# Performance work log

Hardware: AMD Instinct MI355X
Metric: run time of the kernel (lower is better)

The kernel has to match this reference:

```python
import jax, jax.numpy as jnp
from jax import lax
import numpy as np

D, DI, S, K, R = 128, 256, 16, 4, 8  # d_model, d_inner, d_state, d_conv, dt_rank
B, W, N, E = 8, 64, 128, 256


def _ln(x, g, b, eps=1e-5):
    m = x.mean(-1, keepdims=True)
    v = ((x - m) ** 2).mean(-1, keepdims=True)
    return (x - m) * lax.rsqrt(v + eps) * g + b


def _mamba(x, w_in, conv_w, conv_b, w_xp, dt_w, dt_b, Alog, Dp, w_out):
    # x: (Bq, W, D) -> (Bq, W, D). Faithful mamba_ssm.Mamba math (selective scan).
    Bq, Wlen, _ = x.shape
    xz = x @ w_in                       # (Bq, W, 2*DI)
    xc, z = jnp.split(xz, 2, axis=-1)
    # causal depthwise conv over time
    xt = xc.transpose(0, 2, 1)          # (Bq, DI, W)
    xt = lax.conv_general_dilated(xt, conv_w[:, None, :], (1,), [(K - 1, 0)],
                                  feature_group_count=DI)
    xc = jax.nn.silu(xt + conv_b[None, :, None]).transpose(0, 2, 1)  # (Bq, W, DI)
    dbc = xc @ w_xp                     # (Bq, W, R+2S)
    dt = jax.nn.softplus(dbc[..., :R] @ dt_w + dt_b)   # (Bq, W, DI)
    Bm = dbc[..., R:R + S]              # (Bq, W, S)
    Cm = dbc[..., R + S:]               # (Bq, W, S)
    A = -jnp.exp(Alog)                  # (DI, S)

    def step(h, inp):
        dt_t, B_t, C_t, x_t = inp       # (Bq,DI),(Bq,S),(Bq,S),(Bq,DI)
        dA = jnp.exp(dt_t[..., None] * A)                 # (Bq,DI,S)
        h = dA * h + (dt_t * x_t)[..., None] * B_t[:, None, :]
        y = jnp.einsum('bds,bs->bd', h, C_t)
        return h, y

    h0 = jnp.zeros((Bq, DI, S), x.dtype)
    _, ys = lax.scan(step, h0, (dt.transpose(1, 0, 2), Bm.transpose(1, 0, 2),
                                Cm.transpose(1, 0, 2), xc.transpose(1, 0, 2)))
    y = ys.transpose(1, 0, 2) + xc * Dp          # D skip connection
    y = y * jax.nn.silu(z)
    return y @ w_out


def _forward(x_node, x_trace, x_log, mp_in, mp_conv_w, mp_conv_b, mp_xproj,
             mp_dt_w, mp_dt_b, mp_Alog, mp_D, mp_out, mix_w, mix_b,
             an_g, an_b, ff1_w, ff1_b, ff2_w, ff2_b, fln_g, fln_b):
    Bz, Wz, Nz, _ = x_node.shape
    Ez = x_trace.shape[2]
    # (B,W,N,D) -> (B*N, W, D) per-entity temporal sequences
    sn = x_node.transpose(0, 2, 1, 3).reshape(Bz * Nz, Wz, D)
    st = x_trace.transpose(0, 2, 1, 3).reshape(Bz * Ez, Wz, D)
    sl = x_log.transpose(0, 2, 1, 3).reshape(Bz * Nz, Wz, D)

    def mam(i, s):
        return _mamba(s, mp_in[i], mp_conv_w[i], mp_conv_b[i], mp_xproj[i],
                      mp_dt_w[i], mp_dt_b[i], mp_Alog[i], mp_D[i], mp_out[i])

    yn, yt, yl = mam(0, sn), mam(1, st), mam(2, sl)

    # cross-modal mixing of node & log with residual (dropout = identity in eval)
    cat = jnp.concatenate([yn, yl], axis=-1)          # (B*N, W, 2D)
    cat = cat + jax.nn.silu(cat @ mix_w + mix_b)
    yn, yl = jnp.split(cat, 2, axis=-1)

    # back to (B, W, N/E, D)
    yn = yn.reshape(Bz, Nz, Wz, D).transpose(0, 2, 1, 3)
    yt = yt.reshape(Bz, Ez, Wz, D).transpose(0, 2, 1, 3)
    yl = yl.reshape(Bz, Nz, Wz, D).transpose(0, 2, 1, 3)

    # AddALL: AddNorm(old, new) = LN(dropout(new) + old)
    n1 = _ln(yn + x_node, an_g[0], an_b[0])
    t1 = _ln(yt + x_trace, an_g[1], an_b[1])
    l1 = _ln(yl + x_log, an_g[2], an_b[2])

    # FFN: AddNorm(x, FeedForward(x)) per modality, LeakyReLU(0.01)
    def ffn(i, x):
        h = jax.nn.leaky_relu(x @ ff1_w[i] + ff1_b[i], 0.01)
        return _ln(h @ ff2_w[i] + ff2_b[i] + x, fln_g[i], fln_b[i])

    n2, t2, l2 = ffn(0, n1), ffn(1, t1), ffn(2, l1)
    # concat along entity axis (all feature dims = D) for a single output
    return jnp.concatenate([n2, t2, l2], axis=2)      # (B, W, 2N+E, D)


def setup_inputs() -> dict:
    key = jax.random.key(0)
    ks = jax.random.split(key, 16)
    f = lambda k, shp, s=1.0: jax.random.normal(k, shp, dtype=jnp.float32) * s
    return {
        'x_node': f(ks[0], (B, W, N, D)),
        'x_trace': f(ks[1], (B, W, E, D)),
        'x_log': f(ks[2], (B, W, N, D)),
        'mp_in': f(ks[3], (3, D, 2 * DI), 0.05),
        'mp_conv_w': f(ks[4], (3, DI, K), 0.2),
        'mp_conv_b': jnp.zeros((3, DI), jnp.float32),
        'mp_xproj': f(ks[5], (3, DI, R + 2 * S), 0.05),
        'mp_dt_w': f(ks[6], (3, R, DI), 0.1),
        'mp_dt_b': jnp.full((3, DI), float(np.log(np.expm1(0.01))), jnp.float32),
        'mp_Alog': jnp.log(jnp.broadcast_to(jnp.arange(1, S + 1, dtype=jnp.float32), (3, DI, S))),
        'mp_D': jnp.ones((3, DI), jnp.float32),
        'mp_out': f(ks[7], (3, DI, D), 0.05),
        'mix_w': f(ks[8], (2 * D, 2 * D), 0.05),
        'mix_b': jnp.zeros((2 * D,), jnp.float32),
        'an_g': jnp.ones((3, D), jnp.float32),
        'an_b': jnp.zeros((3, D), jnp.float32),
        'ff1_w': f(ks[9], (3, D, 4 * D), 0.05),
        'ff1_b': jnp.zeros((3, 4 * D), jnp.float32),
        'ff2_w': f(ks[10], (3, 4 * D, D), 0.05),
        'ff2_b': jnp.zeros((3, D), jnp.float32),
        'fln_g': jnp.ones((3, D), jnp.float32),
        'fln_b': jnp.zeros((3, D), jnp.float32),
    }


def reference(x_node, x_trace, x_log, mp_in, mp_conv_w, mp_conv_b, mp_xproj,
              mp_dt_w, mp_dt_b, mp_Alog, mp_D, mp_out, mix_w, mix_b,
              an_g, an_b, ff1_w, ff1_b, ff2_w, ff2_b, fln_g, fln_b):
    return _forward(x_node, x_trace, x_log, mp_in, mp_conv_w, mp_conv_b,
                    mp_xproj, mp_dt_w, mp_dt_b, mp_Alog, mp_D, mp_out,
                    mix_w, mix_b, an_g, an_b, ff1_w, ff1_b, ff2_w, ff2_b,
                    fln_g, fln_b)
```

## Files before the change

kernel.cpp:

```cpp
#include <hip/hip_runtime.h>
#include <hip/hip_bf16.h>

#define DEV __device__ __forceinline__

typedef __attribute__((ext_vector_type(8))) short bf16x8;
typedef __attribute__((ext_vector_type(4))) float f32x4;
typedef __attribute__((ext_vector_type(2))) float f32x2;

DEV f32x4 MF(bf16x8 a, bf16x8 b, f32x4 c) {
  return __builtin_amdgcn_mfma_f32_16x16x32_bf16(a, b, c, 0, 0, 0);
}

DEV float bf2f(unsigned short u) {
  union { unsigned int i; float f; } v; v.i = ((unsigned int)u) << 16; return v.f;
}
DEV unsigned short f2bf(float f) {
  __hip_bfloat16 h = __float2bfloat16(f);
  unsigned short r; __builtin_memcpy(&r, &h, 2); return r;
}
DEV unsigned int packbf(float a, float b) {
  float2 p; p.x = a; p.y = b;
  __hip_bfloat162 h = __float22bfloat162_rn(p);
  unsigned int r; __builtin_memcpy(&r, &h, 4); return r;
}
#define LOG2E 1.442695041f
#define LN2   0.6931471806f
DEV float silu_fast(float v) {
  float e = __builtin_amdgcn_exp2f(v * -LOG2E);
  return v * __builtin_amdgcn_rcpf(1.f + e);
}
DEV float softplus_fast(float v) {
  float e = __builtin_amdgcn_exp2f(v * LOG2E);
  float l = __builtin_amdgcn_logf(1.f + e) * LN2;
  return v > 15.f ? v : l;
}

#define WS_WINT   0
#define WS_WXPT   196608
#define WS_WOUTT  233472
#define WS_FF1T   331776
#define WS_FF2T   528384
#define WS_MIXT   724992
#define WS_TOTAL  790528

__global__ __launch_bounds__(256) void prep_kernel(
    const float* __restrict__ w_in, const float* __restrict__ w_xp,
    const float* __restrict__ w_out, const float* __restrict__ ff1,
    const float* __restrict__ ff2, const float* __restrict__ mixw,
    unsigned short* __restrict__ ws)
{
  int idx = blockIdx.x * 256 + threadIdx.x;
  if (idx >= WS_TOTAL) return;
  float v;
  if (idx < WS_WXPT) {
    int j = idx, s = j / 65536, r = j % 65536, n = r >> 7, k = r & 127;
    v = w_in[s * 65536 + k * 512 + n];
  } else if (idx < WS_WOUTT) {
    int j = idx - WS_WXPT, s = j / 12288, r = j % 12288, n = r >> 8, k = r & 255;
    v = (n < 40) ? w_xp[s * 10240 + k * 40 + n] : 0.f;
  } else if (idx < WS_FF1T) {
    int j = idx - WS_WOUTT, s = j / 32768, r = j % 32768, n = r >> 8, k = r & 255;
    v = w_out[s * 32768 + k * 128 + n];
  } else if (idx < WS_FF2T) {
    int j = idx - WS_FF1T, s = j / 65536, r = j % 65536, n = r >> 7, k = r & 127;
    v = ff1[s * 65536 + k * 512 + n];
  } else if (idx < WS_MIXT) {
    int j = idx - WS_FF2T, s = j / 65536, r = j % 65536, n = r >> 9, k = r & 511;
    v = ff2[s * 65536 + k * 128 + n];
  } else {
    int j = idx - WS_MIXT, n = j >> 8, k = j & 255;
    v = mixw[k * 256 + n];
  }
  ws[idx] = f2bf(v);
}

__global__ __launch_bounds__(256, 2) void mamba_front(
    const float* __restrict__ xn, const float* __restrict__ xt,
    const float* __restrict__ xl,
    const unsigned short* __restrict__ w_inT_all,
    const float* __restrict__ conv_w_all, const float* __restrict__ conv_b_all,
    const unsigned short* __restrict__ w_xpT_all,
    const float* __restrict__ dt_w_all, const float* __restrict__ dt_b_all,
    const float* __restrict__ Alog_all, const float* __restrict__ Dp_all,
    const unsigned short* __restrict__ w_outT_all,
    const float* __restrict__ an_g, const float* __restrict__ an_b,
    const unsigned short* __restrict__ ff1T, const float* __restrict__ fb1,
    const unsigned short* __restrict__ ff2T, const float* __restrict__ fb2,
    const float* __restrict__ fln_g, const float* __restrict__ fln_b,
    float* __restrict__ out)
{
  __shared__ __attribute__((aligned(16))) unsigned short xcz[64 * 512];
  __shared__ __attribute__((aligned(16))) char aux[16384];
  unsigned short* xs = (unsigned short*)aux;
  float* dbc = (float*)aux;

  const int tid = threadIdx.x;
  const int lane = tid & 63;
  const int wv = tid >> 6;
  const int lr = lane & 15;
  const int kg = lane >> 4;

  int blk = blockIdx.x, s, q;
  if (blk < 2048)      { s = 1; q = blk; }
  else if (blk < 3072) { s = 0; q = blk - 2048; }
  else                 { s = 2; q = blk - 3072; }
  const int SEQ = (s == 1) ? 256 : 128;
  const int slot_base = (s == 0) ? 0 : (s == 1 ? 128 : 384);
  const float* x = (s == 0) ? xn : (s == 1 ? xt : xl);
  const unsigned short* w_inT  = w_inT_all  + (size_t)s * 65536;
  const unsigned short* w_xpT  = w_xpT_all  + (size_t)s * 12288;
  const unsigned short* w_outT = w_outT_all + (size_t)s * 32768;
  const float* conv_w = conv_w_all + s * 1024;
  const float* conv_b = conv_b_all + s * 256;
  const float* dt_w   = dt_w_all + s * 2048;
  const float* dt_b   = dt_b_all + s * 256;
  const float* Alog   = Alog_all + s * 4096;
  const float* Dp     = Dp_all + s * 256;

  const int b = q / SEQ, n = q - b * SEQ;
  const float* xb = x + ((size_t)b * 64 * SEQ + n) * 128;

  for (int idx = tid; idx < 2048; idx += 256) {
    int t = idx >> 5, qd = (idx & 31) << 2;
    float4 v = *(const float4*)(xb + (size_t)t * SEQ * 128 + qd);
    uint2 p;
    p.x = packbf(v.x, v.y);
    p.y = packbf(v.z, v.w);
    *(uint2*)(&xs[t * 128 + (qd ^ ((t & 7) << 3))]) = p;
  }
  __syncthreads();

  {
    bf16x8 bx[4][4];
#pragma unroll
    for (int jt = 0; jt < 4; ++jt)
#pragma unroll
      for (int ks = 0; ks < 4; ++ks) {
        int t = jt * 16 + lr;
        bx[jt][ks] = *(const bf16x8*)(&xs[t * 128 + ((ks * 32 + kg * 8) ^ ((t & 7) << 3))]);
      }
    const int nb = wv * 128;
#pragma unroll
    for (int at = 0; at < 8; ++at) {
      bf16x8 av[4];
      int arow = nb + at * 16 + lr;
#pragma unroll
      for (int ks = 0; ks < 4; ++ks)
        av[ks] = *(const bf16x8*)(w_inT + arow * 128 + ks * 32 + kg * 8);
#pragma unroll
      for (int jt = 0; jt < 4; ++jt) {
        f32x4 c = {0.f, 0.f, 0.f, 0.f};
#pragma unroll
        for (int ks = 0; ks < 4; ++ks) c = MF(av[ks], bx[jt][ks], c);
        int t = jt * 16 + lr;
        int n0 = nb + at * 16 + kg * 4;
        uint2 p;
        p.x = packbf(c[0], c[1]);
        p.y = packbf(c[2], c[3]);
        *(uint2*)(&xcz[t * 512 + (n0 ^ ((t & 7) << 3))]) = p;
      }
    }
  }
  __syncthreads();

  {
    const int d = tid;
    float cw0 = conv_w[d * 4 + 0], cw1 = conv_w[d * 4 + 1];
    float cw2 = conv_w[d * 4 + 2], cw3 = conv_w[d * 4 + 3];
    float cb = conv_b[d];
    float xm3 = 0.f, xm2 = 0.f, xm1 = 0.f;
    for (int c0 = 0; c0 < 64; c0 += 16) {
      float xv[16];
#pragma unroll
      for (int u = 0; u < 16; ++u) {
        int t = c0 + u;
        xv[u] = bf2f(xcz[t * 512 + (d ^ ((t & 7) << 3))]);
      }
#pragma unroll
      for (int u = 0; u < 16; ++u) {
        float sv = fmaf(cw0, xm3, fmaf(cw1, xm2, fmaf(cw2, xm1, fmaf(cw3, xv[u], cb))));
        xm3 = xm2; xm2 = xm1; xm1 = xv[u];
        xv[u] = silu_fast(sv);
      }
#pragma unroll
      for (int u = 0; u < 16; ++u) {
        int t = c0 + u;
        xcz[t * 512 + (d ^ ((t & 7) << 3))] = f2bf(xv[u]);
      }
    }
  }
  __syncthreads();

  {
    bf16x8 av[8];
    int ta = wv * 16 + lr;
#pragma unroll
    for (int ks = 0; ks < 8; ++ks)
      av[ks] = *(const bf16x8*)(&xcz[ta * 512 + ((ks * 32 + kg * 8) ^ ((ta & 7) << 3))]);
#pragma unroll
    for (int ct = 0; ct < 3; ++ct) {
      f32x4 c = {0.f, 0.f, 0.f, 0.f};
#pragma unroll
      for (int ks = 0; ks < 8; ++ks) {
        bf16x8 bv = *(const bf16x8*)(w_xpT + (ct * 16 + lr) * 256 + ks * 32 + kg * 8);
        c = MF(av[ks], bv, c);
      }
      int tt = wv * 16 + kg * 4;
#pragma unroll
      for (int r = 0; r < 4; ++r)
        dbc[(tt + r) * 48 + ct * 16 + lr] = c[r];
    }
  }
  __syncthreads();

  {
    const int d = tid;
    float dtw[8];
#pragma unroll
    for (int r = 0; r < 8; ++r) dtw[r] = dt_w[r * 256 + d];
    const float dtb = dt_b[d];
    float Af2[16];
#pragma unroll
    for (int s2 = 0; s2 < 16; ++s2)
      Af2[s2] = -__builtin_amdgcn_exp2f(Alog[d * 16 + s2] * LOG2E) * LOG2E;
    const float af0l2 = Af2[0];
    bool geo = true;
#pragma unroll
    for (int s2 = 1; s2 < 16; ++s2)
      geo = geo && (fabsf(Af2[s2] - (float)(s2 + 1) * af0l2) <= 2e-4f * fabsf(Af2[s2]));
    const float Dv = Dp[d];

    const int eoff = d;
    const int zoff = 256 + d;

    if (geo) {
      f32x2 h2[8];
#pragma unroll
      for (int k = 0; k < 8; ++k) h2[k] = (f32x2){0.f, 0.f};
#pragma unroll 2
      for (int t = 0; t < 64; ++t) {
        const f32x4* dr4 = (const f32x4*)&dbc[t * 48];
        f32x4 d0 = dr4[0], d1 = dr4[1];
        float dtv = dtb;
        dtv = fmaf(dtw[0], d0[0], dtv); dtv = fmaf(dtw[1], d0[1], dtv);
        dtv = fmaf(dtw[2], d0[2], dtv); dtv = fmaf(dtw[3], d0[3], dtv);
        dtv = fmaf(dtw[4], d1[0], dtv); dtv = fmaf(dtw[5], d1[1], dtv);
        dtv = fmaf(dtw[6], d1[2], dtv); dtv = fmaf(dtw[7], d1[3], dtv);
        dtv = softplus_fast(dtv);
        int sw = (t & 7) << 3;
        int e = t * 512 + (eoff ^ sw);
        float xv = bf2f(xcz[e]);
        float zf = bf2f(xcz[t * 512 + (zoff ^ sw)]);
        float cf = dtv * xv;
        float r1 = __builtin_amdgcn_exp2f(dtv * af0l2);
        float r2 = r1 * r1;
        f32x2 r2v = {r2, r2};
        f32x2 pp = {r1, r2};
        f32x2 cf2 = {cf, cf};
        f32x2 y2 = {0.f, 0.f};
        f32x4 B0 = dr4[2], B1 = dr4[3], B2 = dr4[4], B3 = dr4[5];
        f32x4 C0 = dr4[6], C1 = dr4[7], C2 = dr4[8], C3 = dr4[9];
        f32x2 Bv[8] = {{B0[0],B0[1]},{B0[2],B0[3]},{B1[0],B1[1]},{B1[2],B1[3]},
                       {B2[0],B2[1]},{B2[2],B2[3]},{B3[0],B3[1]},{B3[2],B3[3]}};
        f32x2 Cv[8] = {{C0[0],C0[1]},{C0[2],C0[3]},{C1[0],C1[1]},{C1[2],C1[3]},
                       {C2[0],C2[1]},{C2[2],C2[3]},{C3[0],C3[1]},{C3[2],C3[3]}};
#pragma unroll
        for (int k = 0; k < 8; ++k) {
          h2[k] = __builtin_elementwise_fma(pp, h2[k], cf2 * Bv[k]);
          y2 = __builtin_elementwise_fma(h2[k], Cv[k], y2);
          pp = pp * r2v;
        }
        float y = y2[0] + y2[1];
        xcz[e] = f2bf((fmaf(xv, Dv, y)) * silu_fast(zf));
      }
    } else {
      float h[16];
#pragma unroll
      for (int s2 = 0; s2 < 16; ++s2) h[s2] = 0.f;
#pragma unroll 2
      for (int t = 0; t < 64; ++t) {
        const float* dr = &dbc[t * 48];
        float dtv = dtb;
#pragma unroll
        for (int r = 0; r < 8; ++r) dtv = fmaf(dtw[r], dr[r], dtv);
        dtv = softplus_fast(dtv);
        int sw = (t & 7) << 3;
        int e = t * 512 + (eoff ^ sw);
        float xv = bf2f(xcz[e]);
        float zf = bf2f(xcz[t * 512 + (zoff ^ sw)]);
        float cf = dtv * xv;
        float y = 0.f;
#pragma unroll
        for (int s2 = 0; s2 < 16; ++s2) {
          float dA = __builtin_amdgcn_exp2f(dtv * Af2[s2]);
          h[s2] = fmaf(dA, h[s2], cf * dr[8 + s2]);
          y = fmaf(h[s2], dr[24 + s2], y);
        }
        xcz[e] = f2bf((fmaf(xv, Dv, y)) * silu_fast(zf));
      }
    }
  }
  __syncthreads();

  {
    bf16x8 av[8];
    int ta = wv * 16 + lr;
#pragma unroll
    for (int ks = 0; ks < 8; ++ks)
      av[ks] = *(const bf16x8*)(&xcz[ta * 512 + ((ks * 32 + kg * 8) ^ ((ta & 7) << 3))]);
    f32x4 acc[8];
#pragma unroll
    for (int ct = 0; ct < 8; ++ct) {
      f32x4 c = {0.f, 0.f, 0.f, 0.f};
#pragma unroll
      for (int ks = 0; ks < 8; ++ks) {
        bf16x8 bv = *(const bf16x8*)(w_outT + (ct * 16 + lr) * 256 + ks * 32 + kg * 8);
        c = MF(av[ks], bv, c);
      }
      acc[ct] = c;
    }
    size_t ob = (size_t)b * 64 * 512 * 128 + (size_t)(slot_base + n) * 128;
    const int trow = wv * 16 + kg * 4;
    if (s != 1) {
#pragma unroll
      for (int ct = 0; ct < 8; ++ct) {
        int cc = ct * 16 + lr;
#pragma unroll
        for (int r = 0; r < 4; ++r)
          out[ob + (size_t)(trow + r) * 65536 + cc] = acc[ct][r];
      }
    } else {
      float sum[4] = {0.f, 0.f, 0.f, 0.f}, sq[4] = {0.f, 0.f, 0.f, 0.f};
#pragma unroll
      for (int ct = 0; ct < 8; ++ct) {
        int col = ct * 16 + lr;
#pragma unroll
        for (int r = 0; r < 4; ++r) {
          int t = trow + r;
          float xr = xb[(size_t)t * SEQ * 128 + col];
          float v = acc[ct][r] + xr;
          acc[ct][r] = v;
          sum[r] += v; sq[r] += v * v;
        }
      }
      float mn[4], rstd[4];
#pragma unroll
      for (int r = 0; r < 4; ++r) {
        float s1 = sum[r], s2 = sq[r];
        s1 += __shfl_xor(s1, 1); s2 += __shfl_xor(s2, 1);
        s1 += __shfl_xor(s1, 2); s2 += __shfl_xor(s2, 2);
        s1 += __shfl_xor(s1, 4); s2 += __shfl_xor(s2, 4);
        s1 += __shfl_xor(s1, 8); s2 += __shfl_xor(s2, 8);
        float mean = s1 * (1.f / 128.f);
        float var = s2 * (1.f / 128.f) - mean * mean;
        mn[r] = mean;
        rstd[r] = rsqrtf(var + 1e-5f);
      }
      const float* G  = an_g + 128;
      const float* Bv = an_b + 128;
#pragma unroll
      for (int ct = 0; ct < 8; ++ct) {
        int col = ct * 16 + lr;
        float gc = G[col], bc = Bv[col];
#pragma unroll
        for (int r = 0; r < 4; ++r) {
          int t = trow + r;
          float t1 = (acc[ct][r] - mn[r]) * rstd[r] * gc + bc;
          xs[t * 128 + (col ^ ((t & 7) << 3))] = f2bf(t1);
        }
      }
      __syncthreads();

      const unsigned short* F1 = ff1T + 65536;
      const unsigned short* F2 = ff2T + 65536;
      const float* B1 = fb1 + 512;
      const float* B2 = fb2 + 128;
      const float* FG = fln_g + 128;
      const float* FB = fln_b + 128;
      {
        bf16x8 bx[4][4];
#pragma unroll
        for (int jt = 0; jt < 4; ++jt)
#pragma unroll
          for (int ks = 0; ks < 4; ++ks) {
            int t = jt * 16 + lr;
            bx[jt][ks] = *(const bf16x8*)(&xs[t * 128 + ((ks * 32 + kg * 8) ^ ((t & 7) << 3))]);
          }
        const int nb = wv * 128;
#pragma unroll
        for (int at = 0; at < 8; ++at) {
          bf16x8 av1[4];
          int arow = nb + at * 16 + lr;
#pragma unroll
          for (int ks = 0; ks < 4; ++ks)
            av1[ks] = *(const bf16x8*)(F1 + arow * 128 + ks * 32 + kg * 8);
          float4 bias = *(const float4*)(B1 + nb + at * 16 + kg * 4);
#pragma unroll
          for (int jt = 0; jt < 4; ++jt) {
            f32x4 c = {0.f, 0.f, 0.f, 0.f};
#pragma unroll
            for (int ks = 0; ks < 4; ++ks) c = MF(av1[ks], bx[jt][ks], c);
            float v0 = c[0] + bias.x; v0 = v0 > 0.f ? v0 : 0.01f * v0;
            float v1 = c[1] + bias.y; v1 = v1 > 0.f ? v1 : 0.01f * v1;
            float v2 = c[2] + bias.z; v2 = v2 > 0.f ? v2 : 0.01f * v2;
            float v3 = c[3] + bias.w; v3 = v3 > 0.f ? v3 : 0.01f * v3;
            int t = jt * 16 + lr;
            int n0 = nb + at * 16 + kg * 4;
            uint2 p;
            p.x = packbf(v0, v1);
            p.y = packbf(v2, v3);
            *(uint2*)(&xcz[t * 512 + (n0 ^ ((t & 7) << 3))]) = p;
          }
        }
      }
      __syncthreads();
      {
        bf16x8 av2[16];
        int ta2 = wv * 16 + lr;
#pragma unroll
        for (int ks = 0; ks < 16; ++ks)
          av2[ks] = *(const bf16x8*)(&xcz[ta2 * 512 + ((ks * 32 + kg * 8) ^ ((ta2 & 7) << 3))]);
        f32x4 a2[8];
#pragma unroll
        for (int ct = 0; ct < 8; ++ct) {
          f32x4 c = {0.f, 0.f, 0.f, 0.f};
#pragma unroll
          for (int ks = 0; ks < 16; ++ks) {
            bf16x8 bv = *(const bf16x8*)(F2 + (ct * 16 + lr) * 512 + ks * 32 + kg * 8);
            c = MF(av2[ks], bv, c);
          }
          a2[ct] = c;
        }
        float vv[8][4];
        float su[4] = {0.f, 0.f, 0.f, 0.f}, sb[4] = {0.f, 0.f, 0.f, 0.f};
#pragma unroll
        for (int ct = 0; ct < 8; ++ct) {
          int col = ct * 16 + lr;
          float b2c = B2[col];
#pragma unroll
          for (int r = 0; r < 4; ++r) {
            int t = trow + r;
            float xr = bf2f(xs[t * 128 + (col ^ ((t & 7) << 3))]);
            float val = a2[ct][r] + b2c + xr;
            vv[ct][r] = val;
            su[r] += val; sb[r] += val * val;
          }
        }
        float mn2[4], rs2[4];
#pragma unroll
        for (int r = 0; r < 4; ++r) {
          float s1 = su[r], s2 = sb[r];
          s1 += __shfl_xor(s1, 1); s2 += __shfl_xor(s2, 1);
          s1 += __shfl_xor(s1, 2); s2 += __shfl_xor(s2, 2);
          s1 += __shfl_xor(s1, 4); s2 += __shfl_xor(s2, 4);
          s1 += __shfl_xor(s1, 8); s2 += __shfl_xor(s2, 8);
          float mean = s1 * (1.f / 128.f);
          float var = s2 * (1.f / 128.f) - mean * mean;
          mn2[r] = mean;
          rs2[r] = rsqrtf(var + 1e-5f);
        }
#pragma unroll
        for (int ct = 0; ct < 8; ++ct) {
          int col = ct * 16 + lr;
          float gc = FG[col], bc = FB[col];
#pragma unroll
          for (int r = 0; r < 4; ++r)
            out[ob + (size_t)(trow + r) * 65536 + col] = (vv[ct][r] - mn2[r]) * rs2[r] * gc + bc;
        }
      }
    }
  }
}

__global__ __launch_bounds__(256, 2) void mix_ffn_kernel(
    float* __restrict__ out, const unsigned short* __restrict__ mixT,
    const float* __restrict__ mix_b,
    const float* __restrict__ xn, const float* __restrict__ xl,
    const float* __restrict__ an_g, const float* __restrict__ an_b,
    const unsigned short* __restrict__ ff1T, const float* __restrict__ fb1,
    const unsigned short* __restrict__ ff2T, const float* __restrict__ fb2,
    const float* __restrict__ fln_g, const float* __restrict__ fln_b)
{
  __shared__ __attribute__((aligned(16))) unsigned short cs[64 * 256];
  __shared__ __attribute__((aligned(16))) unsigned short xs[64 * 128];
  __shared__ __attribute__((aligned(16))) unsigned short hT[64 * 256];

  const int tid = threadIdx.x;
  const int lane = tid & 63;
  const int wv = tid >> 6;
  const int lr = lane & 15;
  const int kg = lane >> 4;
  const int bn = blockIdx.x;
  const int b = bn >> 7, n = bn & 127;
  const size_t base_n = (((size_t)b * 64) * 512 + n) * 128;
  const size_t base_l = (((size_t)b * 64) * 512 + 384 + n) * 128;

  for (int idx = tid; idx < 4096; idx += 256) {
    int t = idx >> 6, r = idx & 63;
    int half = r >> 5, qd = (r & 31) << 2;
    const float* src = out + (half ? base_l : base_n) + (size_t)t * 65536 + qd;
    float4 v = *(const float4*)src;
    int col = half * 128 + qd;
    uint2 p;
    p.x = packbf(v.x, v.y);
    p.y = packbf(v.z, v.w);
    *(uint2*)(&cs[t * 256 + (col ^ ((t & 7) << 3))]) = p;
  }
  __syncthreads();

  bf16x8 av[8];
  int ta = wv * 16 + lr;
#pragma unroll
  for (int ks = 0; ks < 8; ++ks)
    av[ks] = *(const bf16x8*)(&cs[ta * 256 + ((ks * 32 + kg * 8) ^ ((ta & 7) << 3))]);

  const int trow = wv * 16 + kg * 4;
#pragma unroll
  for (int half = 0; half < 2; ++half) {
    const int sf = half ? 2 : 0;
    const float* xres_base = half ? xl : xn;
    f32x4 acc[8];
#pragma unroll
    for (int ct = 0; ct < 8; ++ct) {
      f32x4 c = {0.f, 0.f, 0.f, 0.f};
      int colg = half * 128 + ct * 16 + lr;
#pragma unroll
      for (int ks = 0; ks < 8; ++ks) {
        bf16x8 bv = *(const bf16x8*)(mixT + colg * 256 + ks * 32 + kg * 8);
        c = MF(av[ks], bv, c);
      }
      acc[ct] = c;
    }
    float sum[4] = {0.f, 0.f, 0.f, 0.f}, sq[4] = {0.f, 0.f, 0.f, 0.f};
#pragma unroll
    for (int ct = 0; ct < 8; ++ct) {
      int col = ct * 16 + lr;
      int colg = half * 128 + col;
      float bcol = mix_b[colg];
#pragma unroll
      for (int r = 0; r < 4; ++r) {
        int t = trow + r;
        float orig = bf2f(cs[t * 256 + (colg ^ ((t & 7) << 3))]);
        float xr = xres_base[(((size_t)b * 64 + t) * 128 + n) * 128 + col];
        float v = orig + silu_fast(acc[ct][r] + bcol) + xr;
        acc[ct][r] = v;
        sum[r] += v; sq[r] += v * v;
      }
    }
    float mn[4], rstd[4];
#pragma unroll
    for (int r = 0; r < 4; ++r) {
      float s1 = sum[r], s2 = sq[r];
      s1 += __shfl_xor(s1, 1); s2 += __shfl_xor(s2, 1);
      s1 += __shfl_xor(s1, 2); s2 += __shfl_xor(s2, 2);
      s1 += __shfl_xor(s1, 4); s2 += __shfl_xor(s2, 4);
      s1 += __shfl_xor(s1, 8); s2 += __shfl_xor(s2, 8);
      float mean = s1 * (1.f / 128.f);
      float var = s2 * (1.f / 128.f) - mean * mean;
      mn[r] = mean;
      rstd[r] = rsqrtf(var + 1e-5f);
    }
    {
      const float* G  = an_g + (half ? 256 : 0);
      const float* Bv = an_b + (half ? 256 : 0);
#pragma unroll
      for (int ct = 0; ct < 8; ++ct) {
        int col = ct * 16 + lr;
        float gc = G[col], bc = Bv[col];
#pragma unroll
        for (int r = 0; r < 4; ++r) {
          int t = trow + r;
          float n1 = (acc[ct][r] - mn[r]) * rstd[r] * gc + bc;
          xs[t * 128 + (col ^ ((t & 7) << 3))] = f2bf(n1);
        }
      }
    }
    __syncthreads();

    const unsigned short* F1 = ff1T + (size_t)sf * 65536;
    const unsigned short* F2 = ff2T + (size_t)sf * 65536;
    const float* B1 = fb1 + sf * 512;
    const float* B2 = fb2 + sf * 128;
    const float* FG = fln_g + sf * 128;
    const float* FB = fln_b + sf * 128;

    bf16x8 bx[4][4];
#pragma unroll
    for (int jt = 0; jt < 4; ++jt)
#pragma unroll
      for (int ks = 0; ks < 4; ++ks) {
        int t = jt * 16 + lr;
        bx[jt][ks] = *(const bf16x8*)(&xs[t * 128 + ((ks * 32 + kg * 8) ^ ((t & 7) << 3))]);
      }

    f32x4 acc2[8];
#pragma unroll
    for (int ct = 0; ct < 8; ++ct) acc2[ct] = (f32x4){0.f, 0.f, 0.f, 0.f};

#pragma unroll
    for (int kh = 0; kh < 2; ++kh) {
      const int nb = kh * 256 + wv * 64;
#pragma unroll
      for (int at = 0; at < 4; ++at) {
        bf16x8 av1[4];
        int arow = nb + at * 16 + lr;
#pragma unroll
        for (int ks = 0; ks < 4; ++ks)
          av1[ks] = *(const bf16x8*)(F1 + arow * 128 + ks * 32 + kg * 8);
        float4 bias = *(const float4*)(B1 + nb + at * 16 + kg * 4);
#pragma unroll
        for (int jt = 0; jt < 4; ++jt) {
          f32x4 c = {0.f, 0.f, 0.f, 0.f};
#pragma unroll
          for (int ks = 0; ks < 4; ++ks) c = MF(av1[ks], bx[jt][ks], c);
          float v0 = c[0] + bias.x; v0 = v0 > 0.f ? v0 : 0.01f * v0;
          float v1 = c[1] + bias.y; v1 = v1 > 0.f ? v1 : 0.01f * v1;
          float v2 = c[2] + bias.z; v2 = v2 > 0.f ? v2 : 0.01f * v2;
          float v3 = c[3] + bias.w; v3 = v3 > 0.f ? v3 : 0.01f * v3;
          int t = jt * 16 + lr;
          int nl = wv * 64 + at * 16 + kg * 4;
          uint2 p;
          p.x = packbf(v0, v1);
          p.y = packbf(v2, v3);
          *(uint2*)(&hT[t * 256 + (nl ^ ((t & 7) << 3))]) = p;
        }
      }
      __syncthreads();

      bf16x8 av2[8];
#pragma unroll
      for (int ks = 0; ks < 8; ++ks)
        av2[ks] = *(const bf16x8*)(&hT[ta * 256 + ((ks * 32 + kg * 8) ^ ((ta & 7) << 3))]);
#pragma unroll
      for (int ct = 0; ct < 8; ++ct) {
        f32x4 c = acc2[ct];
#pragma unroll
        for (int ks = 0; ks < 8; ++ks) {
          bf16x8 bv = *(const bf16x8*)(F2 + (ct * 16 + lr) * 512 + kh * 256 + ks * 32 + kg * 8);
          c = MF(av2[ks], bv, c);
        }
        acc2[ct] = c;
      }
      __syncthreads();
    }

    {
      float vv[8][4];
      float su[4] = {0.f, 0.f, 0.f, 0.f}, sb[4] = {0.f, 0.f, 0.f, 0.f};
#pragma unroll
      for (int ct = 0; ct < 8; ++ct) {
        int col = ct * 16 + lr;
        float b2c = B2[col];
#pragma unroll
        for (int r = 0; r < 4; ++r) {
          int t = trow + r;
          float xr = bf2f(xs[t * 128 + (col ^ ((t & 7) << 3))]);
          float val = acc2[ct][r] + b2c + xr;
          vv[ct][r] = val;
          su[r] += val; sb[r] += val * val;
        }
      }
      float mn2[4], rs2[4];
#pragma unroll
      for (int r = 0; r < 4; ++r) {
        float s1 = su[r], s2 = sb[r];
        s1 += __shfl_xor(s1, 1); s2 += __shfl_xor(s2, 1);
        s1 += __shfl_xor(s1, 2); s2 += __shfl_xor(s2, 2);
        s1 += __shfl_xor(s1, 4); s2 += __shfl_xor(s2, 4);
        s1 += __shfl_xor(s1, 8); s2 += __shfl_xor(s2, 8);
        float mean = s1 * (1.f / 128.f);
        float var = s2 * (1.f / 128.f) - mean * mean;
        mn2[r] = mean;
        rs2[r] = rsqrtf(var + 1e-5f);
      }
      size_t base = half ? base_l : base_n;
#pragma unroll
      for (int ct = 0; ct < 8; ++ct) {
        int col = ct * 16 + lr;
        float gc = FG[col], bc = FB[col];
#pragma unroll
        for (int r = 0; r < 4; ++r)
          out[base + (size_t)(trow + r) * 65536 + col] = (vv[ct][r] - mn2[r]) * rs2[r] * gc + bc;
      }
    }
    __syncthreads();
  }
}

extern "C" void kernel_launch(void* const* d_in, const int* in_sizes, int n_in,
                              void* d_out, int out_size, void* d_ws, size_t ws_size,
                              hipStream_t stream) {
  (void)in_sizes; (void)n_in; (void)out_size; (void)ws_size;
  const float* x_node  = (const float*)d_in[0];
  const float* x_trace = (const float*)d_in[1];
  const float* x_log   = (const float*)d_in[2];
  const float* mp_in     = (const float*)d_in[3];
  const float* mp_conv_w = (const float*)d_in[4];
  const float* mp_conv_b = (const float*)d_in[5];
  const float* mp_xproj  = (const float*)d_in[6];
  const float* mp_dt_w   = (const float*)d_in[7];
  const float* mp_dt_b   = (const float*)d_in[8];
  const float* mp_Alog   = (const float*)d_in[9];
  const float* mp_D      = (const float*)d_in[10];
  const float* mp_out    = (const float*)d_in[11];
  const float* mix_w = (const float*)d_in[12];
  const float* mix_b = (const float*)d_in[13];
  const float* an_g  = (const float*)d_in[14];
  const float* an_b  = (const float*)d_in[15];
  const float* ff1_w = (const float*)d_in[16];
  const float* ff1_b = (const float*)d_in[17];
  const float* ff2_w = (const float*)d_in[18];
  const float* ff2_b = (const float*)d_in[19];
  const float* fln_g = (const float*)d_in[20];
  const float* fln_b = (const float*)d_in[21];
  float* out = (float*)d_out;

  unsigned short* ws = (unsigned short*)d_ws;

  prep_kernel<<<(WS_TOTAL + 255) / 256, 256, 0, stream>>>(
      mp_in, mp_xproj, mp_out, ff1_w, ff2_w, mix_w, ws);

  mamba_front<<<4096, 256, 0, stream>>>(
      x_node, x_trace, x_log,
      ws + WS_WINT, mp_conv_w, mp_conv_b, ws + WS_WXPT,
      mp_dt_w, mp_dt_b, mp_Alog, mp_D, ws + WS_WOUTT,
      an_g, an_b,
      ws + WS_FF1T, ff1_b, ws + WS_FF2T, ff2_b, fln_g, fln_b,
      out);

  mix_ffn_kernel<<<1024, 256, 0, stream>>>(
      out, ws + WS_MIXT, mix_b, x_node, x_log, an_g, an_b,
      ws + WS_FF1T, ff1_b, ws + WS_FF2T, ff2_b, fln_g, fln_b);
}
```

Before: 799.3 us.

## Fuse node/log mamba passes with mix-FFN into a single kernel

The mamba front kernel and the mix/FFN kernel are merged. Blocks handling node and log sequences now run both mamba passes for the same (b,n) in sequence, keep the concatenated results in shared memory, and then apply the mix layer and FFN directly. This removes the round trip of those intermediates through global memory and one kernel launch. The cost is that these 1024 blocks each carry two serial passes, which can cause load imbalance against the 2048 single-pass trace blocks, and shared memory is reused, which risks aliasing hazards.

```diff
diff --git a/kernel.cpp b/kernel.cpp
--- a/kernel.cpp
+++ b/kernel.cpp
@@ -74,7 +74,7 @@
   ws[idx] = f2bf(v);
 }
 
-__global__ __launch_bounds__(256, 2) void mamba_front(
+__global__ __launch_bounds__(256, 2) void mamba_all(
     const float* __restrict__ xn, const float* __restrict__ xt,
     const float* __restrict__ xl,
     const unsigned short* __restrict__ w_inT_all,
@@ -83,6 +83,7 @@
     const float* __restrict__ dt_w_all, const float* __restrict__ dt_b_all,
     const float* __restrict__ Alog_all, const float* __restrict__ Dp_all,
     const unsigned short* __restrict__ w_outT_all,
+    const unsigned short* __restrict__ mixT, const float* __restrict__ mix_b,
     const float* __restrict__ an_g, const float* __restrict__ an_b,
     const unsigned short* __restrict__ ff1T, const float* __restrict__ fb1,
     const unsigned short* __restrict__ ff2T, const float* __restrict__ fb2,
@@ -93,428 +94,423 @@
   __shared__ __attribute__((aligned(16))) char aux[16384];
   unsigned short* xs = (unsigned short*)aux;
   float* dbc = (float*)aux;
+  unsigned short* cs = xcz;
+  unsigned short* hT2 = xcz + 64 * 256;
 
   const int tid = threadIdx.x;
   const int lane = tid & 63;
   const int wv = tid >> 6;
   const int lr = lane & 15;
   const int kg = lane >> 4;
-
-  int blk = blockIdx.x, s, q;
-  if (blk < 2048)      { s = 1; q = blk; }
-  else if (blk < 3072) { s = 0; q = blk - 2048; }
-  else                 { s = 2; q = blk - 3072; }
-  const int SEQ = (s == 1) ? 256 : 128;
-  const int slot_base = (s == 0) ? 0 : (s == 1 ? 128 : 384);
-  const float* x = (s == 0) ? xn : (s == 1 ? xt : xl);
-  const unsigned short* w_inT  = w_inT_all  + (size_t)s * 65536;
-  const unsigned short* w_xpT  = w_xpT_all  + (size_t)s * 12288;
-  const unsigned short* w_outT = w_outT_all + (size_t)s * 32768;
-  const float* conv_w = conv_w_all + s * 1024;
-  const float* conv_b = conv_b_all + s * 256;
-  const float* dt_w   = dt_w_all + s * 2048;
-  const float* dt_b   = dt_b_all + s * 256;
-  const float* Alog   = Alog_all + s * 4096;
-  const float* Dp     = Dp_all + s * 256;
-
-  const int b = q / SEQ, n = q - b * SEQ;
-  const float* xb = x + ((size_t)b * 64 * SEQ + n) * 128;
-
-  for (int idx = tid; idx < 2048; idx += 256) {
-    int t = idx >> 5, qd = (idx & 31) << 2;
-    float4 v = *(const float4*)(xb + (size_t)t * SEQ * 128 + qd);
-    uint2 p;
-    p.x = packbf(v.x, v.y);
-    p.y = packbf(v.z, v.w);
-    *(uint2*)(&xs[t * 128 + (qd ^ ((t & 7) << 3))]) = p;
-  }
-  __syncthreads();
-
-  {
-    bf16x8 bx[4][4];
-#pragma unroll
-    for (int jt = 0; jt < 4; ++jt)
-#pragma unroll
-      for (int ks = 0; ks < 4; ++ks) {
-        int t = jt * 16 + lr;
-        bx[jt][ks] = *(const bf16x8*)(&xs[t * 128 + ((ks * 32 + kg * 8) ^ ((t & 7) << 3))]);
-      }
-    const int nb = wv * 128;
-#pragma unroll
-    for (int at = 0; at < 8; ++at) {
-      bf16x8 av[4];
-      int arow = nb + at * 16 + lr;
-#pragma unroll
-      for (int ks = 0; ks < 4; ++ks)
-        av[ks] = *(const bf16x8*)(w_inT + arow * 128 + ks * 32 + kg * 8);
-#pragma unroll
-      for (int jt = 0; jt < 4; ++jt) {
+  const int trow = wv * 16 + kg * 4;
+  const int ta = wv * 16 + lr;
+
+  const bool is_double = blockIdx.x < 1024;
+  const int npass = is_double ? 2 : 1;
+  int bD = 0, nD = 0, qT = 0;
+  if (is_double) { bD = blockIdx.x >> 7; nD = blockIdx.x & 127; }
+  else           { qT = blockIdx.x - 1024; }
+
+  unsigned int ypk[16];
+
+  for (int p = 0; p < npass; ++p) {
+    int s;
+    const float* x;
+    int SEQ, b, n;
+    if (is_double) {
+      s = (p == 0) ? 0 : 2;
+      x = (p == 0) ? xn : xl;
+      SEQ = 128; b = bD; n = nD;
+    } else {
+      s = 1; x = xt; SEQ = 256; b = qT / 256; n = qT - b * 256;
+    }
+    const unsigned short* w_inT  = w_inT_all  + (size_t)s * 65536;
+    const unsigned short* w_xpT  = w_xpT_all  + (size_t)s * 12288;
+    const unsigned short* w_outT = w_outT_all + (size_t)s * 32768;
+    const float* conv_w = conv_w_all + s * 1024;
+    const float* conv_b = conv_b_all + s * 256;
+    const float* dt_w   = dt_w_all + s * 2048;
+    const float* dt_b   = dt_b_all + s * 256;
+    const float* Alog   = Alog_all + s * 4096;
+    const float* Dp     = Dp_all + s * 256;
+    const float* xb = x + ((size_t)b * 64 * SEQ + n) * 128;
+
+    for (int idx = tid; idx < 2048; idx += 256) {
+      int t = idx >> 5, qd = (idx & 31) << 2;
+      float4 v = *(const float4*)(xb + (size_t)t * SEQ * 128 + qd);
+      uint2 pk;
+      pk.x = packbf(v.x, v.y);
+      pk.y = packbf(v.z, v.w);
+      *(uint2*)(&xs[t * 128 + (qd ^ ((t & 7) << 3))]) = pk;
+    }
+    __syncthreads();
+
+    {
+      bf16x8 bx[4][4];
+#pragma unroll
+      for (int jt = 0; jt < 4; ++jt)
+#pragma unroll
+        for (int ks = 0; ks < 4; ++ks) {
+          int t = jt * 16 + lr;
+          bx[jt][ks] = *(const bf16x8*)(&xs[t * 128 + ((ks * 32 + kg * 8) ^ ((t & 7) << 3))]);
+        }
+      const int nb = wv * 128;
+#pragma unroll
+      for (int at = 0; at < 8; ++at) {
+        bf16x8 av[4];
+        int arow = nb + at * 16 + lr;
+#pragma unroll
+        for (int ks = 0; ks < 4; ++ks)
+          av[ks] = *(const bf16x8*)(w_inT + arow * 128 + ks * 32 + kg * 8);
+#pragma unroll
+        for (int jt = 0; jt < 4; ++jt) {
+          f32x4 c = {0.f, 0.f, 0.f, 0.f};
+#pragma unroll
+          for (int ks = 0; ks < 4; ++ks) c = MF(av[ks], bx[jt][ks], c);
+          int t = jt * 16 + lr;
+          int n0 = nb + at * 16 + kg * 4;
+          uint2 pk;
+          pk.x = packbf(c[0], c[1]);
+          pk.y = packbf(c[2], c[3]);
+          *(uint2*)(&xcz[t * 512 + (n0 ^ ((t & 7) << 3))]) = pk;
+        }
+      }
+    }
+    __syncthreads();
+
+    {
+      const int d = tid;
+      float cw0 = conv_w[d * 4 + 0], cw1 = conv_w[d * 4 + 1];
+      float cw2 = conv_w[d * 4 + 2], cw3 = conv_w[d * 4 + 3];
+      float cb = conv_b[d];
+      float xm3 = 0.f, xm2 = 0.f, xm1 = 0.f;
+      for (int c0 = 0; c0 < 64; c0 += 16) {
+        float xv[16];
+#pragma unroll
+        for (int u = 0; u < 16; ++u) {
+          int t = c0 + u;
+          xv[u] = bf2f(xcz[t * 512 + (d ^ ((t & 7) << 3))]);
+        }
+#pragma unroll
+        for (int u = 0; u < 16; ++u) {
+          float sv = fmaf(cw0, xm3, fmaf(cw1, xm2, fmaf(cw2, xm1, fmaf(cw3, xv[u], cb))));
+          xm3 = xm2; xm2 = xm1; xm1 = xv[u];
+          xv[u] = silu_fast(sv);
+        }
+#pragma unroll
+        for (int u = 0; u < 16; ++u) {
+          int t = c0 + u;
+          xcz[t * 512 + (d ^ ((t & 7) << 3))] = f2bf(xv[u]);
+        }
+      }
+    }
+    __syncthreads();
+
+    {
+      bf16x8 av[8];
+#pragma unroll
+      for (int ks = 0; ks < 8; ++ks)
+        av[ks] = *(const bf16x8*)(&xcz[ta * 512 + ((ks * 32 + kg * 8) ^ ((ta & 7) << 3))]);
+#pragma unroll
+      for (int ct = 0; ct < 3; ++ct) {
         f32x4 c = {0.f, 0.f, 0.f, 0.f};
 #pragma unroll
-        for (int ks = 0; ks < 4; ++ks) c = MF(av[ks], bx[jt][ks], c);
-        int t = jt * 16 + lr;
-        int n0 = nb + at * 16 + kg * 4;
-        uint2 p;
-        p.x = packbf(c[0], c[1]);
-        p.y = packbf(c[2], c[3]);
-        *(uint2*)(&xcz[t * 512 + (n0 ^ ((t & 7) << 3))]) = p;
-      }
-    }
-  }
-  __syncthreads();
-
-  {
-    const int d = tid;
-    float cw0 = conv_w[d * 4 + 0], cw1 = conv_w[d * 4 + 1];
-    float cw2 = conv_w[d * 4 + 2], cw3 = conv_w[d * 4 + 3];
-    float cb = conv_b[d];
-    float xm3 = 0.f, xm2 = 0.f, xm1 = 0.f;
-    for (int c0 = 0; c0 < 64; c0 += 16) {
-      float xv[16];
-#pragma unroll
-      for (int u = 0; u < 16; ++u) {
-        int t = c0 + u;
-        xv[u] = bf2f(xcz[t * 512 + (d ^ ((t & 7) << 3))]);
-      }
-#pragma unroll
-      for (int u = 0; u < 16; ++u) {
-        float sv = fmaf(cw0, xm3, fmaf(cw1, xm2, fmaf(cw2, xm1, fmaf(cw3, xv[u], cb))));
-        xm3 = xm2; xm2 = xm1; xm1 = xv[u];
-        xv[u] = silu_fast(sv);
-      }
-#pragma unroll
-      for (int u = 0; u < 16; ++u) {
-        int t = c0 + u;
-        xcz[t * 512 + (d ^ ((t & 7) << 3))] = f2bf(xv[u]);
-      }
-    }
-  }
-  __syncthreads();
-
-  {
-    bf16x8 av[8];
-    int ta = wv * 16 + lr;
-#pragma unroll
-    for (int ks = 0; ks < 8; ++ks)
-      av[ks] = *(const bf16x8*)(&xcz[ta * 512 + ((ks * 32 + kg * 8) ^ ((ta & 7) << 3))]);
-#pragma unroll
-    for (int ct = 0; ct < 3; ++ct) {
-      f32x4 c = {0.f, 0.f, 0.f, 0.f};
-#pragma unroll
-      for (int ks = 0; ks < 8; ++ks) {
-        bf16x8 bv = *(const bf16x8*)(w_xpT + (ct * 16 + lr) * 256 + ks * 32 + kg * 8);
-        c = MF(av[ks], bv, c);
-      }
-      int tt = wv * 16 + kg * 4;
-#pragma unroll
-      for (int r = 0; r < 4; ++r)
-        dbc[(tt + r) * 48 + ct * 16 + lr] = c[r];
-    }
-  }
-  __syncthreads();
-
-  {
-    const int d = tid;
-    float dtw[8];
-#pragma unroll
-    for (int r = 0; r < 8; ++r) dtw[r] = dt_w[r * 256 + d];
-    const float dtb = dt_b[d];
-    float Af2[16];
-#pragma unroll
-    for (int s2 = 0; s2 < 16; ++s2)
-      Af2[s2] = -__builtin_amdgcn_exp2f(Alog[d * 16 + s2] * LOG2E) * LOG2E;
-    const float af0l2 = Af2[0];
-    bool geo = true;
-#pragma unroll
-    for (int s2 = 1; s2 < 16; ++s2)
-      geo = geo && (fabsf(Af2[s2] - (float)(s2 + 1) * af0l2) <= 2e-4f * fabsf(Af2[s2]));
-    const float Dv = Dp[d];
-
-    const int eoff = d;
-    const int zoff = 256 + d;
-
-    if (geo) {
-      f32x2 h2[8];
-#pragma unroll
-      for (int k = 0; k < 8; ++k) h2[k] = (f32x2){0.f, 0.f};
+        for (int ks = 0; ks < 8; ++ks) {
+          bf16x8 bv = *(const bf16x8*)(w_xpT + (ct * 16 + lr) * 256 + ks * 32 + kg * 8);
+          c = MF(av[ks], bv, c);
+        }
+        int tt = wv * 16 + kg * 4;
+#pragma unroll
+        for (int r = 0; r < 4; ++r)
+          dbc[(tt + r) * 48 + ct * 16 + lr] = c[r];
+      }
+    }
+    __syncthreads();
+
+    {
+      const int d = tid;
+      float dtw[8];
+#pragma unroll
+      for (int r = 0; r < 8; ++r) dtw[r] = dt_w[r * 256 + d];
+      const float dtb = dt_b[d];
+      float Af2[16];
+#pragma unroll
+      for (int s2 = 0; s2 < 16; ++s2)
+        Af2[s2] = -__builtin_amdgcn_exp2f(Alog[d * 16 + s2] * LOG2E) * LOG2E;
+      const float af0l2 = Af2[0];
+      bool geo = true;
+#pragma unroll
+      for (int s2 = 1; s2 < 16; ++s2)
+        geo = geo && (fabsf(Af2[s2] - (float)(s2 + 1) * af0l2) <= 2e-4f * fabsf(Af2[s2]));
+      const float Dv = Dp[d];
+      const int eoff = d;
+      const int zoff = 256 + d;
+
+      if (geo) {
+        f32x2 h2[8];
+#pragma unroll
+        for (int k = 0; k < 8; ++k) h2[k] = (f32x2){0.f, 0.f};
 #pragma unroll 2
-      for (int t = 0; t < 64; ++t) {
-        const f32x4* dr4 = (const f32x4*)&dbc[t * 48];
-        f32x4 d0 = dr4[0], d1 = dr4[1];
-        float dtv = dtb;
-        dtv = fmaf(dtw[0], d0[0], dtv); dtv = fmaf(dtw[1], d0[1], dtv);
-        dtv = fmaf(dtw[2], d0[2], dtv); dtv = fmaf(dtw[3], d0[3], dtv);
-        dtv = fmaf(dtw[4], d1[0], dtv); dtv = fmaf(dtw[5], d1[1], dtv);
-        dtv = fmaf(dtw[6], d1[2], dtv); dtv = fmaf(dtw[7], d1[3], dtv);
-        dtv = softplus_fast(dtv);
-        int sw = (t & 7) << 3;
-        int e = t * 512 + (eoff ^ sw);
-        float xv = bf2f(xcz[e]);
-        float zf = bf2f(xcz[t * 512 + (zoff ^ sw)]);
-        float cf = dtv * xv;
-        float r1 = __builtin_amdgcn_exp2f(dtv * af0l2);
-        float r2 = r1 * r1;
-        f32x2 r2v = {r2, r2};
-        f32x2 pp = {r1, r2};
-        f32x2 cf2 = {cf, cf};
-        f32x2 y2 = {0.f, 0.f};
-        f32x4 B0 = dr4[2], B1 = dr4[3], B2 = dr4[4], B3 = dr4[5];
-        f32x4 C0 = dr4[6], C1 = dr4[7], C2 = dr4[8], C3 = dr4[9];
-        f32x2 Bv[8] = {{B0[0],B0[1]},{B0[2],B0[3]},{B1[0],B1[1]},{B1[2],B1[3]},
-                       {B2[0],B2[1]},{B2[2],B2[3]},{B3[0],B3[1]},{B3[2],B3[3]}};
-        f32x2 Cv[8] = {{C0[0],C0[1]},{C0[2],C0[3]},{C1[0],C1[1]},{C1[2],C1[3]},
-                       {C2[0],C2[1]},{C2[2],C2[3]},{C3[0],C3[1]},{C3[2],C3[3]}};
-#pragma unroll
-        for (int k = 0; k < 8; ++k) {
-          h2[k] = __builtin_elementwise_fma(pp, h2[k], cf2 * Bv[k]);
-          y2 = __builtin_elementwise_fma(h2[k], Cv[k], y2);
-          pp = pp * r2v;
-        }
-        float y = y2[0] + y2[1];
-        xcz[e] = f2bf((fmaf(xv, Dv, y)) * silu_fast(zf));
-      }
-    } else {
-      float h[16];
-#pragma unroll
-      for (int s2 = 0; s2 < 16; ++s2) h[s2] = 0.f;
+        for (int t = 0; t < 64; ++t) {
+          const f32x4* dr4 = (const f32x4*)&dbc[t * 48];
+          f32x4 d0 = dr4[0], d1 = dr4[1];
+          float dtv = dtb;
+          dtv = fmaf(dtw[0], d0[0], dtv); dtv = fmaf(dtw[1], d0[1], dtv);
+          dtv = fmaf(dtw[2], d0[2], dtv); dtv = fmaf(dtw[3], d0[3], dtv);
+          dtv = fmaf(dtw[4], d1[0], dtv); dtv = fmaf(dtw[5], d1[1], dtv);
+          dtv = fmaf(dtw[6], d1[2], dtv); dtv = fmaf(dtw[7], d1[3], dtv);
+          dtv = softplus_fast(dtv);
+          int sw = (t & 7) << 3;
+          int e = t * 512 + (eoff ^ sw);
+          float xv = bf2f(xcz[e]);
+          float zf = bf2f(xcz[t * 512 + (zoff ^ sw)]);
+          float cf = dtv * xv;
+          float r1 = __builtin_amdgcn_exp2f(dtv * af0l2);
+          float r2 = r1 * r1;
+          f32x2 r2v = {r2, r2};
+          f32x2 pp = {r1, r2};
+          f32x2 cf2 = {cf, cf};
+          f32x2 y2 = {0.f, 0.f};
+          f32x4 B0 = dr4[2], B1 = dr4[3], B2 = dr4[4], B3 = dr4[5];
+          f32x4 C0 = dr4[6], C1 = dr4[7], C2 = dr4[8], C3 = dr4[9];
+          f32x2 Bv[8] = {{B0[0],B0[1]},{B0[2],B0[3]},{B1[0],B1[1]},{B1[2],B1[3]},
+                         {B2[0],B2[1]},{B2[2],B2[3]},{B3[0],B3[1]},{B3[2],B3[3]}};
+          f32x2 Cv[8] = {{C0[0],C0[1]},{C0[2],C0[3]},{C1[0],C1[1]},{C1[2],C1[3]},
+                         {C2[0],C2[1]},{C2[2],C2[3]},{C3[0],C3[1]},{C3[2],C3[3]}};
+#pragma unroll
+          for (int k = 0; k < 8; ++k) {
+            h2[k] = __builtin_elementwise_fma(pp, h2[k], cf2 * Bv[k]);
+            y2 = __builtin_elementwise_fma(h2[k], Cv[k], y2);
+            pp = pp * r2v;
+          }
+          float y = y2[0] + y2[1];
+          xcz[e] = f2bf((fmaf(xv, Dv, y)) * silu_fast(zf));
+        }
+      } else {
+        float h[16];
+#pragma unroll
+        for (int s2 = 0; s2 < 16; ++s2) h[s2] = 0.f;
 #pragma unroll 2
-      for (int t = 0; t < 64; ++t) {
-        const float* dr = &dbc[t * 48];
-        float dtv = dtb;
-#pragma unroll
-        for (int r = 0; r < 8; ++r) dtv = fmaf(dtw[r], dr[r], dtv);
-        dtv = softplus_fast(dtv);
-        int sw = (t & 7) << 3;
-        int e = t * 512 + (eoff ^ sw);
-        float xv = bf2f(xcz[e]);
-        float zf = bf2f(xcz[t * 512 + (zoff ^ sw)]);
-        float cf = dtv * xv;
-        float y = 0.f;
-#pragma unroll
-        for (int s2 = 0; s2 < 16; ++s2) {
-          float dA = __builtin_amdgcn_exp2f(dtv * Af2[s2]);
-          h[s2] = fmaf(dA, h[s2], cf * dr[8 + s2]);
-          y = fmaf(h[s2], dr[24 + s2], y);
-        }
-        xcz[e] = f2bf((fmaf(xv, Dv, y)) * silu_fast(zf));
-      }
-    }
-  }
-  __syncthreads();
-
-  {
-    bf16x8 av[8];
-    int ta = wv * 16 + lr;
-#pragma unroll
-    for (int ks = 0; ks < 8; ++ks)
-      av[ks] = *(const bf16x8*)(&xcz[ta * 512 + ((ks * 32 + kg * 8) ^ ((ta & 7) << 3))]);
-    f32x4 acc[8];
-#pragma unroll
-    for (int ct = 0; ct < 8; ++ct) {
-      f32x4 c = {0.f, 0.f, 0.f, 0.f};
-#pragma unroll
-      for (int ks = 0; ks < 8; ++ks) {
-        bf16x8 bv = *(const bf16x8*)(w_outT + (ct * 16 + lr) * 256 + ks * 32 + kg * 8);
-        c = MF(av[ks], bv, c);
-      }
-      acc[ct] = c;
-    }
-    size_t ob = (size_t)b * 64 * 512 * 128 + (size_t)(slot_base + n) * 128;
-    const int trow = wv * 16 + kg * 4;
-    if (s != 1) {
+        for (int t = 0; t < 64; ++t) {
+          const float* dr = &dbc[t * 48];
+          float dtv = dtb;
+#pragma unroll
+          for (int r = 0; r < 8; ++r) dtv = fmaf(dtw[r], dr[r], dtv);
+          dtv = softplus_fast(dtv);
+          int sw = (t & 7) << 3;
+          int e = t * 512 + (eoff ^ sw);
+          float xv = bf2f(xcz[e]);
+          float zf = bf2f(xcz[t * 512 + (zoff ^ sw)]);
+          float cf = dtv * xv;
+          float y = 0.f;
+#pragma unroll
+          for (int s2 = 0; s2 < 16; ++s2) {
+            float dA = __builtin_amdgcn_exp2f(dtv * Af2[s2]);
+            h[s2] = fmaf(dA, h[s2], cf * dr[8 + s2]);
+            y = fmaf(h[s2], dr[24 + s2], y);
+          }
+          xcz[e] = f2bf((fmaf(xv, Dv, y)) * silu_fast(zf));
+        }
+      }
+    }
+    __syncthreads();
+
+    {
+      bf16x8 av[8];
+#pragma unroll
+      for (int ks = 0; ks < 8; ++ks)
+        av[ks] = *(const bf16x8*)(&xcz[ta * 512 + ((ks * 32 + kg * 8) ^ ((ta & 7) << 3))]);
+      f32x4 acc[8];
 #pragma unroll
       for (int ct = 0; ct < 8; ++ct) {
-        int cc = ct * 16 + lr;
-#pragma unroll
-        for (int r = 0; r < 4; ++r)
-          out[ob + (size_t)(trow + r) * 65536 + cc] = acc[ct][r];
-      }
-    } else {
-      float sum[4] = {0.f, 0.f, 0.f, 0.f}, sq[4] = {0.f, 0.f, 0.f, 0.f};
-#pragma unroll
-      for (int ct = 0; ct < 8; ++ct) {
-        int col = ct * 16 + lr;
-#pragma unroll
-        for (int r = 0; r < 4; ++r) {
-          int t = trow + r;
-          float xr = xb[(size_t)t * SEQ * 128 + col];
-          float v = acc[ct][r] + xr;
-          acc[ct][r] = v;
-          sum[r] += v; sq[r] += v * v;
-        }
-      }
-      float mn[4], rstd[4];
-#pragma unroll
-      for (int r = 0; r < 4; ++r) {
-        float s1 = sum[r], s2 = sq[r];
-        s1 += __shfl_xor(s1, 1); s2 += __shfl_xor(s2, 1);
-        s1 += __shfl_xor(s1, 2); s2 += __shfl_xor(s2, 2);
-        s1 += __shfl_xor(s1, 4); s2 += __shfl_xor(s2, 4);
-        s1 += __shfl_xor(s1, 8); s2 += __shfl_xor(s2, 8);
-        float mean = s1 * (1.f / 128.f);
-        float var = s2 * (1.f / 128.f) - mean * mean;
-        mn[r] = mean;
-        rstd[r] = rsqrtf(var + 1e-5f);
-      }
-      const float* G  = an_g + 128;
-      const float* Bv = an_b + 128;
-#pragma unroll
-      for (int ct = 0; ct < 8; ++ct) {
-        int col = ct * 16 + lr;
-        float gc = G[col], bc = Bv[col];
-#pragma unroll
-        for (int r = 0; r < 4; ++r) {
-          int t = trow + r;
-          float t1 = (acc[ct][r] - mn[r]) * rstd[r] * gc + bc;
-          xs[t * 128 + (col ^ ((t & 7) << 3))] = f2bf(t1);
-        }
-      }
-      __syncthreads();
-
-      const unsigned short* F1 = ff1T + 65536;
-      const unsigned short* F2 = ff2T + 65536;
-      const float* B1 = fb1 + 512;
-      const float* B2 = fb2 + 128;
-      const float* FG = fln_g + 128;
-      const float* FB = fln_b + 128;
-      {
-        bf16x8 bx[4][4];
-#pragma unroll
-        for (int jt = 0; jt < 4; ++jt)
-#pragma unroll
-          for (int ks = 0; ks < 4; ++ks) {
-            int t = jt * 16 + lr;
-            bx[jt][ks] = *(const bf16x8*)(&xs[t * 128 + ((ks * 32 + kg * 8) ^ ((t & 7) << 3))]);
-          }
-        const int nb = wv * 128;
-#pragma unroll
-        for (int at = 0; at < 8; ++at) {
-          bf16x8 av1[4];
-          int arow = nb + at * 16 + lr;
-#pragma unroll
-          for (int ks = 0; ks < 4; ++ks)
-            av1[ks] = *(const bf16x8*)(F1 + arow * 128 + ks * 32 + kg * 8);
-          float4 bias = *(const float4*)(B1 + nb + at * 16 + kg * 4);
-#pragma unroll
-          for (int jt = 0; jt < 4; ++jt) {
-            f32x4 c = {0.f, 0.f, 0.f, 0.f};
-#pragma unroll
-            for (int ks = 0; ks < 4; ++ks) c = MF(av1[ks], bx[jt][ks], c);
-            float v0 = c[0] + bias.x; v0 = v0 > 0.f ? v0 : 0.01f * v0;
-            float v1 = c[1] + bias.y; v1 = v1 > 0.f ? v1 : 0.01f * v1;
-            float v2 = c[2] + bias.z; v2 = v2 > 0.f ? v2 : 0.01f * v2;
-            float v3 = c[3] + bias.w; v3 = v3 > 0.f ? v3 : 0.01f * v3;
-            int t = jt * 16 + lr;
-            int n0 = nb + at * 16 + kg * 4;
-            uint2 p;
-            p.x = packbf(v0, v1);
-            p.y = packbf(v2, v3);
-            *(uint2*)(&xcz[t * 512 + (n0 ^ ((t & 7) << 3))]) = p;
-          }
-        }
-      }
-      __syncthreads();
-      {
-        bf16x8 av2[16];
-        int ta2 = wv * 16 + lr;
-#pragma unroll
-        for (int ks = 0; ks < 16; ++ks)
-          av2[ks] = *(const bf16x8*)(&xcz[ta2 * 512 + ((ks * 32 + kg * 8) ^ ((ta2 & 7) << 3))]);
-        f32x4 a2[8];
-#pragma unroll
-        for (int ct = 0; ct < 8; ++ct) {
-          f32x4 c = {0.f, 0.f, 0.f, 0.f};
-#pragma unroll
-          for (int ks = 0; ks < 16; ++ks) {
-            bf16x8 bv = *(const bf16x8*)(F2 + (ct * 16 + lr) * 512 + ks * 32 + kg * 8);
-            c = MF(av2[ks], bv, c);
-          }
-          a2[ct] = c;
-        }
-        float vv[8][4];
-        float su[4] = {0.f, 0.f, 0.f, 0.f}, sb[4] = {0.f, 0.f, 0.f, 0.f};
+        f32x4 c = {0.f, 0.f, 0.f, 0.f};
+#pragma unroll
+        for (int ks = 0; ks < 8; ++ks) {
+          bf16x8 bv = *(const bf16x8*)(w_outT + (ct * 16 + lr) * 256 + ks * 32 + kg * 8);
+          c = MF(av[ks], bv, c);
+        }
+        acc[ct] = c;
+      }
+
+      if (is_double) {
+        if (p == 0) {
+#pragma unroll
+          for (int ct = 0; ct < 8; ++ct) {
+            ypk[ct * 2 + 0] = packbf(acc[ct][0], acc[ct][1]);
+            ypk[ct * 2 + 1] = packbf(acc[ct][2], acc[ct][3]);
+          }
+        } else {
+          __syncthreads();
+#pragma unroll
+          for (int ct = 0; ct < 8; ++ct) {
+            int col = ct * 16 + lr;
+#pragma unroll
+            for (int r = 0; r < 4; ++r) {
+              int t = trow + r;
+              int sw = (t & 7) << 3;
+              unsigned int pk = ypk[ct * 2 + (r >> 1)];
+              unsigned short yn16 = (r & 1) ? (unsigned short)(pk >> 16)
+                                            : (unsigned short)(pk & 0xffff);
+              cs[t * 256 + (col ^ sw)] = yn16;
+              cs[t * 256 + ((128 + col) ^ sw)] = f2bf(acc[ct][r]);
+            }
+          }
+        }
+      } else {
+        const float* xb2 = xt + ((size_t)b * 64 * 256 + n) * 128;
+        size_t ob = (size_t)b * 64 * 512 * 128 + (size_t)(128 + n) * 128;
+        float sum[4] = {0.f, 0.f, 0.f, 0.f}, sq[4] = {0.f, 0.f, 0.f, 0.f};
 #pragma unroll
         for (int ct = 0; ct < 8; ++ct) {
           int col = ct * 16 + lr;
-          float b2c = B2[col];
 #pragma unroll
           for (int r = 0; r < 4; ++r) {
             int t = trow + r;
-            float xr = bf2f(xs[t * 128 + (col ^ ((t & 7) << 3))]);
-            float val = a2[ct][r] + b2c + xr;
-            vv[ct][r] = val;
-            su[r] += val; sb[r] += val * val;
-          }
-        }
-        float mn2[4], rs2[4];
+            float xr = xb2[(size_t)t * 256 * 128 + col];
+            float v = acc[ct][r] + xr;
+            acc[ct][r] = v;
+            sum[r] += v; sq[r] += v * v;
+          }
+        }
+        float mn[4], rstd[4];
 #pragma unroll
         for (int r = 0; r < 4; ++r) {
-          float s1 = su[r], s2 = sb[r];
+          float s1 = sum[r], s2 = sq[r];
           s1 += __shfl_xor(s1, 1); s2 += __shfl_xor(s2, 1);
           s1 += __shfl_xor(s1, 2); s2 += __shfl_xor(s2, 2);
           s1 += __shfl_xor(s1, 4); s2 += __shfl_xor(s2, 4);
           s1 += __shfl_xor(s1, 8); s2 += __shfl_xor(s2, 8);
           float mean = s1 * (1.f / 128.f);
           float var = s2 * (1.f / 128.f) - mean * mean;
-          mn2[r] = mean;
-          rs2[r] = rsqrtf(var + 1e-5f);
-        }
+          mn[r] = mean;
+          rstd[r] = rsqrtf(var + 1e-5f);
+        }
+        const float* G  = an_g + 128;
+        const float* Bv = an_b + 128;
 #pragma unroll
         for (int ct = 0; ct < 8; ++ct) {
           int col = ct * 16 + lr;
-          float gc = FG[col], bc = FB[col];
-#pragma unroll
-          for (int r = 0; r < 4; ++r)
-            out[ob + (size_t)(trow + r) * 65536 + col] = (vv[ct][r] - mn2[r]) * rs2[r] * gc + bc;
+          float gc = G[col], bc = Bv[col];
+#pragma unroll
+          for (int r = 0; r < 4; ++r) {
+            int t = trow + r;
+            float t1 = (acc[ct][r] - mn[r]) * rstd[r] * gc + bc;
+            xs[t * 128 + (col ^ ((t & 7) << 3))] = f2bf(t1);
+          }
+        }
+        __syncthreads();
+
+        const unsigned short* F1 = ff1T + 65536;
+        const unsigned short* F2 = ff2T + 65536;
+        const float* B1 = fb1 + 512;
+        const float* B2 = fb2 + 128;
+        const float* FG = fln_g + 128;
+        const float* FB = fln_b + 128;
+        {
+          bf16x8 bx[4][4];
+#pragma unroll
+          for (int jt = 0; jt < 4; ++jt)
+#pragma unroll
+            for (int ks = 0; ks < 4; ++ks) {
+              int t = jt * 16 + lr;
+              bx[jt][ks] = *(const bf16x8*)(&xs[t * 128 + ((ks * 32 + kg * 8) ^ ((t & 7) << 3))]);
+            }
+          const int nb = wv * 128;
+#pragma unroll
+          for (int at = 0; at < 8; ++at) {
+            bf16x8 av1[4];
+            int arow = nb + at * 16 + lr;
+#pragma unroll
+            for (int ks = 0; ks < 4; ++ks)
+              av1[ks] = *(const bf16x8*)(F1 + arow * 128 + ks * 32 + kg * 8);
+            float4 bias = *(const float4*)(B1 + nb + at * 16 + kg * 4);
+#pragma unroll
+            for (int jt = 0; jt < 4; ++jt) {
+              f32x4 c = {0.f, 0.f, 0.f, 0.f};
+#pragma unroll
+              for (int ks = 0; ks < 4; ++ks) c = MF(av1[ks], bx[jt][ks], c);
+              float v0 = c[0] + bias.x; v0 = v0 > 0.f ? v0 : 0.01f * v0;
+              float v1 = c[1] + bias.y; v1 = v1 > 0.f ? v1 : 0.01f * v1;
+              float v2 = c[2] + bias.z; v2 = v2 > 0.f ? v2 : 0.01f * v2;
+              float v3 = c[3] + bias.w; v3 = v3 > 0.f ? v3 : 0.01f * v3;
+              int t = jt * 16 + lr;
+              int n0 = nb + at * 16 + kg * 4;
+              uint2 pk;
+              pk.x = packbf(v0, v1);
+              pk.y = packbf(v2, v3);
+              *(uint2*)(&xcz[t * 512 + (n0 ^ ((t & 7) << 3))]) = pk;
+            }
+          }
+        }
+        __syncthreads();
+        {
+          bf16x8 av2[16];
+#pragma unroll
+          for (int ks = 0; ks < 16; ++ks)
+            av2[ks] = *(const bf16x8*)(&xcz[ta * 512 + ((ks * 32 + kg * 8) ^ ((ta & 7) << 3))]);
+          f32x4 a2[8];
+#pragma unroll
+          for (int ct = 0; ct < 8; ++ct) {
+            f32x4 c = {0.f, 0.f, 0.f, 0.f};
+#pragma unroll
+            for (int ks = 0; ks < 16; ++ks) {
+              bf16x8 bv = *(const bf16x8*)(F2 + (ct * 16 + lr) * 512 + ks * 32 + kg * 8);
+              c = MF(av2[ks], bv, c);
+            }
+            a2[ct] = c;
+          }
+          float vv[8][4];
+          float su[4] = {0.f, 0.f, 0.f, 0.f}, sb[4] = {0.f, 0.f, 0.f, 0.f};
+#pragma unroll
+          for (int ct = 0; ct < 8; ++ct) {
+            int col = ct * 16 + lr;
+            float b2c = B2[col];
+#pragma unroll
+            for (int r = 0; r < 4; ++r) {
+              int t = trow + r;
+              float xr = bf2f(xs[t * 128 + (col ^ ((t & 7) << 3))]);
+              float val = a2[ct][r] + b2c + xr;
+              vv[ct][r] = val;
+              su[r] += val; sb[r] += val * val;
+            }
+          }
+          float mn2[4], rs2[4];
+#pragma unroll
+          for (int r = 0; r < 4; ++r) {
+            float s1 = su[r], s2 = sb[r];
+            s1 += __shfl_xor(s1, 1); s2 += __shfl_xor(s2, 1);
+            s1 += __shfl_xor(s1, 2); s2 += __shfl_xor(s2, 2);
+            s1 += __shfl_xor(s1, 4); s2 += __shfl_xor(s2, 4);
+            s1 += __shfl_xor(s1, 8); s2 += __shfl_xor(s2, 8);
+            float mean = s1 * (1.f / 128.f);
+            float var = s2 * (1.f / 128.f) - mean * mean;
+            mn2[r] = mean;
+            rs2[r] = rsqrtf(var + 1e-5f);
+          }
+#pragma unroll
+          for (int ct = 0; ct < 8; ++ct) {
+            int col = ct * 16 + lr;
+            float gc = FG[col], bc = FB[col];
+#pragma unroll
+            for (int r = 0; r < 4; ++r)
+              out[ob + (size_t)(trow + r) * 65536 + col] = (vv[ct][r] - mn2[r]) * rs2[r] * gc + bc;
+          }
         }
       }
     }
   }
-}
-
-__global__ __launch_bounds__(256, 2) void mix_ffn_kernel(
-    float* __restrict__ out, const unsigned short* __restrict__ mixT,
-    const float* __restrict__ mix_b,
-    const float* __restrict__ xn, const float* __restrict__ xl,
-    const float* __restrict__ an_g, const float* __restrict__ an_b,
-    const unsigned short* __restrict__ ff1T, const float* __restrict__ fb1,
-    const unsigned short* __restrict__ ff2T, const float* __restrict__ fb2,
-    const float* __restrict__ fln_g, const float* __restrict__ fln_b)
-{
-  __shared__ __attribute__((aligned(16))) unsigned short cs[64 * 256];
-  __shared__ __attribute__((aligned(16))) unsigned short xs[64 * 128];
-  __shared__ __attribute__((aligned(16))) unsigned short hT[64 * 256];
-
-  const int tid = threadIdx.x;
-  const int lane = tid & 63;
-  const int wv = tid >> 6;
-  const int lr = lane & 15;
-  const int kg = lane >> 4;
-  const int bn = blockIdx.x;
-  const int b = bn >> 7, n = bn & 127;
-  const size_t base_n = (((size_t)b * 64) * 512 + n) * 128;
-  const size_t base_l = (((size_t)b * 64) * 512 + 384 + n) * 128;
-
-  for (int idx = tid; idx < 4096; idx += 256) {
-    int t = idx >> 6, r = idx & 63;
-    int half = r >> 5, qd = (r & 31) << 2;
-    const float* src = out + (half ? base_l : base_n) + (size_t)t * 65536 + qd;
-    float4 v = *(const float4*)src;
-    int col = half * 128 + qd;
-    uint2 p;
-    p.x = packbf(v.x, v.y);
-    p.y = packbf(v.z, v.w);
-    *(uint2*)(&cs[t * 256 + (col ^ ((t & 7) << 3))]) = p;
-  }
+
+  if (!is_double) return;
+
   __syncthreads();
+  const size_t base_n = (((size_t)bD * 64) * 512 + nD) * 128;
+  const size_t base_l = (((size_t)bD * 64) * 512 + 384 + nD) * 128;
 
   bf16x8 av[8];
-  int ta = wv * 16 + lr;
 #pragma unroll
   for (int ks = 0; ks < 8; ++ks)
     av[ks] = *(const bf16x8*)(&cs[ta * 256 + ((ks * 32 + kg * 8) ^ ((ta & 7) << 3))]);
 
-  const int trow = wv * 16 + kg * 4;
 #pragma unroll
   for (int half = 0; half < 2; ++half) {
     const int sf = half ? 2 : 0;
@@ -541,7 +537,7 @@
       for (int r = 0; r < 4; ++r) {
         int t = trow + r;
         float orig = bf2f(cs[t * 256 + (colg ^ ((t & 7) << 3))]);
-        float xr = xres_base[(((size_t)b * 64 + t) * 128 + n) * 128 + col];
+        float xr = xres_base[(((size_t)bD * 64 + t) * 128 + nD) * 128 + col];
         float v = orig + silu_fast(acc[ct][r] + bcol) + xr;
         acc[ct][r] = v;
         sum[r] += v; sq[r] += v * v;
@@ -619,10 +615,10 @@
           float v3 = c[3] + bias.w; v3 = v3 > 0.f ? v3 : 0.01f * v3;
           int t = jt * 16 + lr;
           int nl = wv * 64 + at * 16 + kg * 4;
-          uint2 p;
-          p.x = packbf(v0, v1);
-          p.y = packbf(v2, v3);
-          *(uint2*)(&hT[t * 256 + (nl ^ ((t & 7) << 3))]) = p;
+          uint2 pk;
+          pk.x = packbf(v0, v1);
+          pk.y = packbf(v2, v3);
+          *(uint2*)(&hT2[t * 256 + (nl ^ ((t & 7) << 3))]) = pk;
         }
       }
       __syncthreads();
@@ -630,7 +626,7 @@
       bf16x8 av2[8];
 #pragma unroll
       for (int ks = 0; ks < 8; ++ks)
-        av2[ks] = *(const bf16x8*)(&hT[ta * 256 + ((ks * 32 + kg * 8) ^ ((ta & 7) << 3))]);
+        av2[ks] = *(const bf16x8*)(&hT2[ta * 256 + ((ks * 32 + kg * 8) ^ ((ta & 7) << 3))]);
 #pragma unroll
       for (int ct = 0; ct < 8; ++ct) {
         f32x4 c = acc2[ct];
@@ -720,15 +716,11 @@
   prep_kernel<<<(WS_TOTAL + 255) / 256, 256, 0, stream>>>(
       mp_in, mp_xproj, mp_out, ff1_w, ff2_w, mix_w, ws);
 
-  mamba_front<<<4096, 256, 0, stream>>>(
+  mamba_all<<<3072, 256, 0, stream>>>(
       x_node, x_trace, x_log,
       ws + WS_WINT, mp_conv_w, mp_conv_b, ws + WS_WXPT,
       mp_dt_w, mp_dt_b, mp_Alog, mp_D, ws + WS_WOUTT,
-      an_g, an_b,
+      ws + WS_MIXT, mix_b, an_g, an_b,
       ws + WS_FF1T, ff1_b, ws + WS_FF2T, ff2_b, fln_g, fln_b,
       out);
-
-  mix_ffn_kernel<<<1024, 256, 0, stream>>>(
-      out, ws + WS_MIXT, mix_b, x_node, x_log, an_g, an_b,
-      ws + WS_FF1T, ff1_b, ws + WS_FF2T, ff2_b, fln_g, fln_b);
-}
+}
```

Result: slower. 1.375 ms (+72.1%).
